# Optimization experiments

Hardware: AMD Instinct MI355X
Metric: run time of the kernel (lower is better)

The kernel has to match this reference:

```python
import jax, jax.numpy as jnp
import numpy as np

KS, AS = 13, 12  # kernel_size (12 vertices + center), anchor_size (icosahedron vertices)


def _icosa():
    # Icosahedron oriented with vertex 0 on +z (required by sort_level_vs xy-rotation logic)
    r5 = np.sqrt(5.0); rr = 2.0 / r5
    vs = [[0.0, 0.0, 1.0]]
    for k in range(5):
        t = 2.0 * np.pi * k / 5.0
        vs.append([rr * np.cos(t), rr * np.sin(t), 1.0 / r5])
    for k in range(5):
        t = 2.0 * np.pi * k / 5.0 + np.pi / 5.0
        vs.append([rr * np.cos(t), rr * np.sin(t), -1.0 / r5])
    vs.append([0.0, 0.0, -1.0])
    return np.array(vs)


def _rotm(axis, ang):
    a = np.asarray(axis, dtype=np.float64); a = a / np.linalg.norm(a)
    K = np.array([[0, -a[2], a[1]], [a[2], 0, -a[0]], [-a[1], a[0], 0]])
    return np.eye(3) + np.sin(ang) * K + (1.0 - np.cos(ang)) * (K @ K)


def _ico_group(vs):
    # Generate the 60-element icosahedral rotation group by closure from two generators
    gens = [_rotm([0.0, 0.0, 1.0], 2 * np.pi / 5), _rotm(vs[1], 2 * np.pi / 5)]
    group = [np.eye(3)]
    keys = {tuple(np.round(np.eye(3), 4).ravel())}
    frontier = [np.eye(3)]
    while frontier:
        nxt = []
        for g in frontier:
            for h in gens:
                c = h @ g
                k = tuple(np.round(c, 4).ravel())
                if k not in keys:
                    keys.add(k); group.append(c); nxt.append(c)
        frontier = nxt
    return group


def _sort_level_vs(v_idxs, vs):
    # Faithful port of sort_level_vs: order ring vertices by successive 72-deg xy rotations
    out = [v_idxs[0]]
    vs_l = vs[v_idxs][:, :2]
    cur = vs_l[[0]]
    dth = 2 * np.pi / 5
    R = np.array([[np.cos(dth), -np.sin(dth)], [np.sin(dth), np.cos(dth)]])
    for _ in range(4):
        cur = R.dot(cur.T).T
        out.append(v_idxs[np.argmin(np.abs(vs_l - cur).sum(1))])
    return np.array(out)


def _build_buffers():
    vs = _icosa()
    dots = vs @ vs.T
    v0_adjs = np.where(np.abs(dots[0] - 1.0 / np.sqrt(5)) < 1e-6)[0]
    v0_lv2 = np.where(np.abs(dots[0] + 1.0 / np.sqrt(5)) < 1e-6)[0]
    v0_opp = int(np.argmin(dots[0]))
    # 12 rotation anchors: one group element mapping vertex 0 to each vertex
    group = _ico_group(vs)
    vRs = []
    for i in range(12):
        for R in group:
            if np.linalg.norm(R @ vs[0] - vs[i]) < 1e-5:
                vRs.append(R); break
    vRs = np.stack(vRs)  # [12,3,3]
    rot_v = np.einsum('rij,aj->rai', vRs, vs)  # [12,12,3]
    d = np.linalg.norm(rot_v[:, :, None, :] - vs[None, None], axis=-1)
    trace_idx_ori = np.argmin(d, axis=2)  # [12,12] vertex permutation per anchor rotation
    trace_idx_rot = np.empty_like(trace_idx_ori)
    for r in range(12):
        trace_idx_rot[r, trace_idx_ori[r]] = np.arange(12)
    trace_idxv_rot = np.concatenate([trace_idx_rot, np.full((12, 1), 12, np.int64)], axis=1)  # [12,13]
    # idx_map: faithful port of the __init__ construction (maps 13*12 slots -> 36 weight params)
    inv = np.empty(12, np.int64)
    inv[0] = 0; inv[v0_adjs] = 1; inv[v0_lv2] = 2; inv[v0_opp] = 3
    a_s = _sort_level_vs(v0_adjs, vs)
    l_s = _sort_level_vs(v0_lv2, vs)
    idx_map = np.empty(KS * AS, np.int64)
    idx_map[:AS] = inv
    idx_map[v0_opp * AS:(v0_opp + 1) * AS] = inv + 4
    idx_map[-AS:] = inv + 8
    seq1 = np.arange(12, 24); seq2 = np.arange(24, 36)
    idx_map[a_s[0] * AS:(a_s[0] + 1) * AS] = seq1
    idx_map[l_s[0] * AS:(l_s[0] + 1) * AS] = seq2
    shifts = [[4, 0, 1, 2, 3], [3, 4, 0, 1, 2], [2, 3, 4, 0, 1], [1, 2, 3, 4, 0]]
    for j, sh in enumerate(shifts, start=1):
        new = np.empty(12, np.int64)
        new[a_s] = a_s[sh]; new[l_s] = l_s[sh]
        new[0] = 0; new[v0_opp] = v0_opp
        idx_map[a_s[j] * AS:(a_s[j] + 1) * AS] = seq1[new]
        idx_map[l_s[j] * AS:(l_s[j] + 1) * AS] = seq2[new]
    return idx_map, trace_idxv_rot, trace_idx_rot


def setup_inputs() -> dict:
    key = jax.random.key(0)
    k1, k2 = jax.random.split(key)
    B, CIN, COUT, P = 8, 16, 16, 4096
    x = jax.random.normal(k1, (B, CIN, KS, P, AS), dtype=jnp.float32)
    W = jax.random.normal(k2, (COUT, CIN, 36), dtype=jnp.float32) * 0.05  # xavier-scale
    idx_map, tivr, tir = _build_buffers()
    return {
        'x': x,
        'W': W,
        'idx_map': jnp.asarray(idx_map, jnp.int32),
        'trace_idxv_rot': jnp.asarray(tivr, jnp.int32),
        'trace_idx_rot': jnp.asarray(tir, jnp.int32),
    }


def reference(x, W, idx_map, trace_idxv_rot, trace_idx_rot):
    d_out, d_in, _ = W.shape
    # Expand 36 free params to the [d, c, k, a] kernel via idx_map gather
    Wm = W[:, :, idx_map].reshape(d_out, d_in, KS, AS)
    # The two torch.gather calls (dims 2 then 3) collapse to:
    # Wfull[d,c,k,a,r] = Wm[d,c, trace_idxv_rot[r,k], trace_idx_rot[r,a]]
    Wfull = Wm[:, :, trace_idxv_rot[:, :, None], trace_idx_rot[:, None, :]]  # [d,c,r,k,a]
    return jnp.einsum('dcrka,bckpa->bdpr', Wfull, x)
```

## Files before the change

### kernel.cpp

```cpp
#include <hip/hip_runtime.h>

#define B_    8
#define CIN_  16
#define COUT_ 16
#define KS_   13
#define AS_   12
#define P_    4096
#define R_    12
#define M_    192
#define KTOT  2496
#define BN    128
#define KT    96
#define NSTEP 26
#define LDP   104

typedef float  f32x4  __attribute__((ext_vector_type(4)));
typedef __bf16 bf16x4 __attribute__((ext_vector_type(4)));
typedef __bf16 bf16x8 __attribute__((ext_vector_type(8)));

__global__ void build_wmatf(const float* __restrict__ W,
                            const int* __restrict__ idx_map,
                            const int* __restrict__ tivr,
                            const int* __restrict__ tir,
                            __bf16* __restrict__ WmatF) {
  int gid  = blockIdx.x * blockDim.x + threadIdx.x;
  int lane = gid & 63;
  int fid  = gid >> 6;
  int kt   = fid / 36;
  int rem  = fid - kt * 36;
  int mt   = rem / 3;
  int ks   = rem - mt * 3;

  int row = mt * 16 + (lane & 15);
  int d = row / R_;
  int r = row - d * R_;

  bf16x8 v;
#pragma unroll
  for (int e = 0; e < 8; ++e) {
    int kap = kt * KT + ks * 32 + (lane >> 4) * 8 + e;
    int c = kap / (KS_ * AS_);
    int t = kap - c * (KS_ * AS_);
    int k = t / AS_;
    int a = t - k * AS_;
    int s = idx_map[tivr[r * KS_ + k] * AS_ + tir[r * AS_ + a]];
    v[e] = (__bf16)W[(d * CIN_ + c) * 36 + s];
  }
  *(bf16x8*)(WmatF + (size_t)gid * 8) = v;
}

__global__ __launch_bounds__(512, 2)
void s2conv(const float* __restrict__ x,
            const __bf16* __restrict__ WmatF,
            float* __restrict__ out) {
  __shared__ __bf16 Xs[2][BN][LDP];

  const int tid  = threadIdx.x;
  const int lane = tid & 63;
  const int wave = tid >> 6;
  const int wm   = wave >> 2;
  const int wn   = wave & 3;
  const int l15  = lane & 15;
  const int l4   = lane >> 4;

  const int wg = blockIdx.x;
  const int b  = wg >> 5;
  const int p0 = (wg & 31) << 7;

  f32x4 acc[6][2];
#pragma unroll
  for (int i = 0; i < 6; ++i)
#pragma unroll
    for (int j = 0; j < 2; ++j)
      acc[i][j] = f32x4{0.f, 0.f, 0.f, 0.f};

  auto load_x = [&](int kt, f32x4 (&st)[6]) {
    int ck = kt * 8 + wave;
    const f32x4* bp =
        (const f32x4*)(x + (size_t)(b * 208 + ck) * 49152 + (size_t)p0 * 12);
#pragma unroll
    for (int it = 0; it < 6; ++it) st[it] = bp[it * 64 + lane];
  };

  auto load_a = [&](int kt, bf16x8 (&af)[18]) {
    const char* base = (const char*)WmatF +
        (size_t)(kt * 36 + wm * 18) * 1024 + lane * 16;
#pragma unroll
    for (int f = 0; f < 18; ++f)
      af[f] = *(const bf16x8*)(base + f * 1024);
  };

  auto write_X = [&](int buf, f32x4 (&st)[6]) {
    char* xsb = (char*)&Xs[buf][0][0];
#pragma unroll
    for (int it = 0; it < 6; ++it) {
      int f4i = it * 64 + lane;
      int pl  = f4i / 3;
      int a   = (f4i - pl * 3) * 4;
      bf16x4 v = __builtin_convertvector(st[it], bf16x4);
      *(bf16x4*)(xsb + pl * (LDP * 2) + (wave * 12 + a) * 2) = v;
    }
  };

  auto mfma_step = [&](int buf, bf16x8 (&af)[18]) {
    const __bf16* xsb = &Xs[buf][0][0];
#pragma unroll
    for (int ks = 0; ks < 3; ++ks) {
      const int col = ks * 32 + l4 * 8;
      bf16x8 bfr[2];
#pragma unroll
      for (int nt = 0; nt < 2; ++nt)
        bfr[nt] = *(const bf16x8*)(xsb + (wn * 32 + nt * 16 + l15) * LDP + col);
#pragma unroll
      for (int mt = 0; mt < 6; ++mt)
#pragma unroll
        for (int nt = 0; nt < 2; ++nt)
          acc[mt][nt] = __builtin_amdgcn_mfma_f32_16x16x32_bf16(
              af[mt * 3 + ks], bfr[nt], acc[mt][nt], 0, 0, 0);
    }
  };

  auto barrier = [&]() {
    asm volatile("s_waitcnt lgkmcnt(0)" ::: "memory");
    __builtin_amdgcn_s_barrier();
  };

  f32x4  stA[6], stB[6];
  bf16x8 af[18];
  load_x(0, stA);
  load_x(1, stB);
  write_X(0, stA);
  barrier();

  for (int kt = 0; kt < NSTEP - 2; kt += 2) {
    load_a(kt, af);
    load_x(kt + 2, stA);
    __builtin_amdgcn_sched_barrier(0);
    write_X(1, stB);
    mfma_step(0, af);
    barrier();

    load_a(kt + 1, af);
    load_x(kt + 3, stB);
    __builtin_amdgcn_sched_barrier(0);
    write_X(0, stA);
    mfma_step(1, af);
    barrier();
  }

  load_a(24, af);
  write_X(1, stB);
  mfma_step(0, af);
  barrier();
  load_a(25, af);
  mfma_step(1, af);

#pragma unroll
  for (int mt = 0; mt < 6; ++mt) {
    int mrow0 = wm * 96 + mt * 16 + l4 * 4;
    int d  = mrow0 / 12;
    int r0 = mrow0 - d * 12;
#pragma unroll
    for (int nt = 0; nt < 2; ++nt) {
      int p = p0 + wn * 32 + nt * 16 + l15;
      float* dst = out + (size_t)((b * 16 + d) * 4096 + p) * 12 + r0;
      *(f32x4*)dst = acc[mt][nt];
    }
  }
}

extern "C" void kernel_launch(void* const* d_in, const int* in_sizes, int n_in,
                              void* d_out, int out_size, void* d_ws, size_t ws_size,
                              hipStream_t stream) {
  const float* x       = (const float*)d_in[0];
  const float* W       = (const float*)d_in[1];
  const int*   idx_map = (const int*)d_in[2];
  const int*   tivr    = (const int*)d_in[3];
  const int*   tir     = (const int*)d_in[4];
  float*       out     = (float*)d_out;
  __bf16*      WmatF   = (__bf16*)d_ws;

  build_wmatf<<<dim3(117), dim3(512), 0, stream>>>(W, idx_map, tivr, tir, WmatF);
  s2conv<<<dim3(256), dim3(512), 0, stream>>>(x, WmatF, out);
}
```

Baseline: 82.35 us.

## Stage weights into LDS via global_load_lds and feed x directly from registers

The dataflow is reversed. Weight fragments are now staged into shared memory with direct global-to-LDS loads, double-buffered across K steps. Each wave reads its x fragments straight from global memory into registers and converts them to bf16 in place, which removes the x LDS transpose and write. Each wave owns 16 pixels and all 192 output rows (12 accumulators). The cost is uncoalesced-ish 16-byte x loads with a large stride and more LDS reads of A per MFMA.

```diff
diff --git a/kernel.cpp b/kernel.cpp
--- a/kernel.cpp
+++ b/kernel.cpp
@@ -1,22 +1,22 @@
 #include <hip/hip_runtime.h>
+#include <stdint.h>
 
-#define B_    8
 #define CIN_  16
-#define COUT_ 16
 #define KS_   13
 #define AS_   12
-#define P_    4096
 #define R_    12
-#define M_    192
-#define KTOT  2496
-#define BN    128
 #define KT    96
 #define NSTEP 26
-#define LDP   104
 
 typedef float  f32x4  __attribute__((ext_vector_type(4)));
 typedef __bf16 bf16x4 __attribute__((ext_vector_type(4)));
 typedef __bf16 bf16x8 __attribute__((ext_vector_type(8)));
+
+__device__ static inline void gll16(const void* g, void* l) {
+  __builtin_amdgcn_global_load_lds(
+      (const __attribute__((address_space(1))) uint32_t*)g,
+      (__attribute__((address_space(3))) uint32_t*)l, 16, 0, 0);
+}
 
 __global__ void build_wmatf(const float* __restrict__ W,
                             const int* __restrict__ idx_map,
@@ -28,8 +28,8 @@
   int fid  = gid >> 6;
   int kt   = fid / 36;
   int rem  = fid - kt * 36;
-  int mt   = rem / 3;
-  int ks   = rem - mt * 3;
+  int ks   = rem / 12;
+  int mt   = rem - ks * 12;
 
   int row = mt * 16 + (lane & 15);
   int d = row / R_;
@@ -53,119 +53,116 @@
 void s2conv(const float* __restrict__ x,
             const __bf16* __restrict__ WmatF,
             float* __restrict__ out) {
-  __shared__ __bf16 Xs[2][BN][LDP];
+  __shared__ __bf16 As[2][36 * 512];
 
   const int tid  = threadIdx.x;
   const int lane = tid & 63;
   const int wave = tid >> 6;
-  const int wm   = wave >> 2;
-  const int wn   = wave & 3;
   const int l15  = lane & 15;
   const int l4   = lane >> 4;
 
   const int wg = blockIdx.x;
   const int b  = wg >> 5;
   const int p0 = (wg & 31) << 7;
+  const int p  = p0 + wave * 16 + l15;
 
-  f32x4 acc[6][2];
+  int voff[3][2];
 #pragma unroll
-  for (int i = 0; i < 6; ++i)
+  for (int ks = 0; ks < 3; ++ks)
 #pragma unroll
-    for (int j = 0; j < 2; ++j)
-      acc[i][j] = f32x4{0.f, 0.f, 0.f, 0.f};
+    for (int h = 0; h < 2; ++h) {
+      int kl = ks * 32 + l4 * 8 + h * 4;
+      int ck = kl / 12, a = kl - ck * 12;
+      voff[ks][h] = (ck * 49152 + a + p * 12) * 4;
+    }
+  const char* xb = (const char*)(x + (size_t)b * 208 * 49152);
 
-  auto load_x = [&](int kt, f32x4 (&st)[6]) {
-    int ck = kt * 8 + wave;
-    const f32x4* bp =
-        (const f32x4*)(x + (size_t)(b * 208 + ck) * 49152 + (size_t)p0 * 12);
+  f32x4 acc[12];
 #pragma unroll
-    for (int it = 0; it < 6; ++it) st[it] = bp[it * 64 + lane];
+  for (int i = 0; i < 12; ++i) acc[i] = f32x4{0.f, 0.f, 0.f, 0.f};
+
+  const int fr0 = wave * 4;
+  const int fr4 = 32 + (wave & 3);
+
+  auto stageA = [&](int kt, int buf) {
+    const char* gk = (const char*)WmatF + (size_t)kt * 36864;
+    char* lb = (char*)&As[buf][0];
+#pragma unroll
+    for (int f = 0; f < 4; ++f) {
+      int frag = fr0 + f;
+      gll16(gk + frag * 1024 + lane * 16, lb + frag * 1024);
+    }
+    gll16(gk + fr4 * 1024 + lane * 16, lb + fr4 * 1024);
   };
 
-  auto load_a = [&](int kt, bf16x8 (&af)[18]) {
-    const char* base = (const char*)WmatF +
-        (size_t)(kt * 36 + wm * 18) * 1024 + lane * 16;
+  auto loadB = [&](int kt, f32x4 (&bs)[3][2]) {
+    const char* xk = xb + (size_t)kt * (8 * 49152 * 4);
 #pragma unroll
-    for (int f = 0; f < 18; ++f)
-      af[f] = *(const bf16x8*)(base + f * 1024);
+    for (int ks = 0; ks < 3; ++ks)
+#pragma unroll
+      for (int h = 0; h < 2; ++h)
+        bs[ks][h] = *(const f32x4*)(xk + voff[ks][h]);
   };
 
-  auto write_X = [&](int buf, f32x4 (&st)[6]) {
-    char* xsb = (char*)&Xs[buf][0][0];
+  auto mfma_phase = [&](int buf, f32x4 (&bs)[3][2]) {
+    const char* lb = (const char*)&As[buf][0];
 #pragma unroll
-    for (int it = 0; it < 6; ++it) {
-      int f4i = it * 64 + lane;
-      int pl  = f4i / 3;
-      int a   = (f4i - pl * 3) * 4;
-      bf16x4 v = __builtin_convertvector(st[it], bf16x4);
-      *(bf16x4*)(xsb + pl * (LDP * 2) + (wave * 12 + a) * 2) = v;
+    for (int ks = 0; ks < 3; ++ks) {
+      bf16x4 lo = __builtin_convertvector(bs[ks][0], bf16x4);
+      bf16x4 hi = __builtin_convertvector(bs[ks][1], bf16x4);
+      bf16x8 bfr = __builtin_shufflevector(lo, hi, 0, 1, 2, 3, 4, 5, 6, 7);
+#pragma unroll
+      for (int mt = 0; mt < 12; ++mt) {
+        bf16x8 af = *(const bf16x8*)(lb + (ks * 12 + mt) * 1024 + lane * 16);
+        acc[mt] = __builtin_amdgcn_mfma_f32_16x16x32_bf16(af, bfr, acc[mt],
+                                                          0, 0, 0);
+      }
     }
   };
 
-  auto mfma_step = [&](int buf, bf16x8 (&af)[18]) {
-    const __bf16* xsb = &Xs[buf][0][0];
-#pragma unroll
-    for (int ks = 0; ks < 3; ++ks) {
-      const int col = ks * 32 + l4 * 8;
-      bf16x8 bfr[2];
-#pragma unroll
-      for (int nt = 0; nt < 2; ++nt)
-        bfr[nt] = *(const bf16x8*)(xsb + (wn * 32 + nt * 16 + l15) * LDP + col);
-#pragma unroll
-      for (int mt = 0; mt < 6; ++mt)
-#pragma unroll
-        for (int nt = 0; nt < 2; ++nt)
-          acc[mt][nt] = __builtin_amdgcn_mfma_f32_16x16x32_bf16(
-              af[mt * 3 + ks], bfr[nt], acc[mt][nt], 0, 0, 0);
-    }
-  };
+  f32x4 bsE[3][2], bsO[3][2];
 
-  auto barrier = [&]() {
-    asm volatile("s_waitcnt lgkmcnt(0)" ::: "memory");
+  stageA(0, 0);
+  __builtin_amdgcn_sched_barrier(0);
+  loadB(0, bsE);
+  __builtin_amdgcn_sched_barrier(0);
+  asm volatile("s_waitcnt vmcnt(6)" ::: "memory");
+  __builtin_amdgcn_s_barrier();
+
+#pragma unroll 1
+  for (int j = 0; j < 24; j += 2) {
+    stageA(j + 1, 1);
+    __builtin_amdgcn_sched_barrier(0);
+    loadB(j + 1, bsO);
+    __builtin_amdgcn_sched_barrier(0);
+    mfma_phase(0, bsE);
+    asm volatile("s_waitcnt vmcnt(6)" ::: "memory");
     __builtin_amdgcn_s_barrier();
-  };
 
-  f32x4  stA[6], stB[6];
-  bf16x8 af[18];
-  load_x(0, stA);
-  load_x(1, stB);
-  write_X(0, stA);
-  barrier();
-
-  for (int kt = 0; kt < NSTEP - 2; kt += 2) {
-    load_a(kt, af);
-    load_x(kt + 2, stA);
+    stageA(j + 2, 0);
     __builtin_amdgcn_sched_barrier(0);
-    write_X(1, stB);
-    mfma_step(0, af);
-    barrier();
-
-    load_a(kt + 1, af);
-    load_x(kt + 3, stB);
+    loadB(j + 2, bsE);
     __builtin_amdgcn_sched_barrier(0);
-    write_X(0, stA);
-    mfma_step(1, af);
-    barrier();
+    mfma_phase(1, bsO);
+    asm volatile("s_waitcnt vmcnt(6)" ::: "memory");
+    __builtin_amdgcn_s_barrier();
   }
-
-  load_a(24, af);
-  write_X(1, stB);
-  mfma_step(0, af);
-  barrier();
-  load_a(25, af);
-  mfma_step(1, af);
+  stageA(25, 1);
+  __builtin_amdgcn_sched_barrier(0);
+  loadB(25, bsO);
+  __builtin_amdgcn_sched_barrier(0);
+  mfma_phase(0, bsE);
+  asm volatile("s_waitcnt vmcnt(6)" ::: "memory");
+  __builtin_amdgcn_s_barrier();
+  mfma_phase(1, bsO);
 
 #pragma unroll
-  for (int mt = 0; mt < 6; ++mt) {
-    int mrow0 = wm * 96 + mt * 16 + l4 * 4;
+  for (int mt = 0; mt < 12; ++mt) {
+    int mrow0 = mt * 16 + l4 * 4;
     int d  = mrow0 / 12;
     int r0 = mrow0 - d * 12;
-#pragma unroll
-    for (int nt = 0; nt < 2; ++nt) {
-      int p = p0 + wn * 32 + nt * 16 + l15;
-      float* dst = out + (size_t)((b * 16 + d) * 4096 + p) * 12 + r0;
-      *(f32x4*)dst = acc[mt][nt];
-    }
+    float* dst = out + (size_t)((b * 16 + d) * 4096 + p) * 12 + r0;
+    *(f32x4*)dst = acc[mt];
   }
 }
 
```

New measurement: 78.11 us. 1.05x faster.

## Shrink GEMM tile to 64 points with 4 waves and double-buffered A fragments

Applied to the files above, without the earlier changes.

The main kernel now uses 256-thread blocks, each covering 64 points over all 192 output rows, and launches 512 blocks instead of 256. Each wave owns 48 rows and 4 column tiles, so every wave reads the whole B tile from LDS. The weight fragments are now double-buffered in registers (even/odd sets) so A loads for the next step overlap the current MFMAs. build_wmatf reorders its fragment layout to match the new per-wave A loads. The intent is better occupancy, more blocks across the CUs and lower A-load latency, at the cost of less reuse of each A fragment per block and more A traffic per point.

```diff
diff --git a/kernel.cpp b/kernel.cpp
--- a/kernel.cpp
+++ b/kernel.cpp
@@ -1,15 +1,10 @@
 #include <hip/hip_runtime.h>
+#include <stdint.h>
 
-#define B_    8
 #define CIN_  16
-#define COUT_ 16
 #define KS_   13
 #define AS_   12
-#define P_    4096
 #define R_    12
-#define M_    192
-#define KTOT  2496
-#define BN    128
 #define KT    96
 #define NSTEP 26
 #define LDP   104
@@ -28,8 +23,11 @@
   int fid  = gid >> 6;
   int kt   = fid / 36;
   int rem  = fid - kt * 36;
-  int mt   = rem / 3;
-  int ks   = rem - mt * 3;
+  int w    = rem / 9;
+  int sub  = rem - w * 9;
+  int mtl  = sub / 3;
+  int ks   = sub - mtl * 3;
+  int mt   = w * 3 + mtl;
 
   int row = mt * 16 + (lane & 15);
   int d = row / R_;
@@ -49,74 +47,80 @@
   *(bf16x8*)(WmatF + (size_t)gid * 8) = v;
 }
 
-__global__ __launch_bounds__(512, 2)
+__global__ __launch_bounds__(256, 2)
 void s2conv(const float* __restrict__ x,
             const __bf16* __restrict__ WmatF,
             float* __restrict__ out) {
-  __shared__ __bf16 Xs[2][BN][LDP];
+  __shared__ __bf16 Xs[2][64][LDP];
 
   const int tid  = threadIdx.x;
   const int lane = tid & 63;
   const int wave = tid >> 6;
-  const int wm   = wave >> 2;
-  const int wn   = wave & 3;
   const int l15  = lane & 15;
   const int l4   = lane >> 4;
 
   const int wg = blockIdx.x;
-  const int b  = wg >> 5;
-  const int p0 = (wg & 31) << 7;
+  const int b  = wg >> 6;
+  const int p0 = (wg & 63) << 6;
 
-  f32x4 acc[6][2];
+  f32x4 acc[3][4];
 #pragma unroll
-  for (int i = 0; i < 6; ++i)
+  for (int i = 0; i < 3; ++i)
 #pragma unroll
-    for (int j = 0; j < 2; ++j)
+    for (int j = 0; j < 4; ++j)
       acc[i][j] = f32x4{0.f, 0.f, 0.f, 0.f};
 
-  auto load_x = [&](int kt, f32x4 (&st)[6]) {
-    int ck = kt * 8 + wave;
-    const f32x4* bp =
-        (const f32x4*)(x + (size_t)(b * 208 + ck) * 49152 + (size_t)p0 * 12);
+  const char* aBase = (const char*)WmatF + (size_t)wave * 9216 + lane * 16;
+  auto loadA = [&](int kt, bf16x8 (&af)[9]) {
+    const char* gk = aBase + (size_t)kt * 36864;
 #pragma unroll
-    for (int it = 0; it < 6; ++it) st[it] = bp[it * 64 + lane];
+    for (int f = 0; f < 9; ++f)
+      af[f] = *(const bf16x8*)(gk + f * 1024);
   };
 
-  auto load_a = [&](int kt, bf16x8 (&af)[18]) {
-    const char* base = (const char*)WmatF +
-        (size_t)(kt * 36 + wm * 18) * 1024 + lane * 16;
+  const char* xb = (const char*)x + ((size_t)b * 208) * 49152 * 4
+                   + (size_t)p0 * 48;
+  auto load_x = [&](int kt, f32x4 (&st)[6]) {
 #pragma unroll
-    for (int f = 0; f < 18; ++f)
-      af[f] = *(const bf16x8*)(base + f * 1024);
+    for (int h = 0; h < 2; ++h) {
+      const char* bp = xb + ((size_t)(kt * 8 + wave * 2 + h)) * (49152 * 4);
+#pragma unroll
+      for (int j = 0; j < 3; ++j)
+        st[h * 3 + j] = *(const f32x4*)(bp + (j * 64 + lane) * 16);
+    }
   };
 
   auto write_X = [&](int buf, f32x4 (&st)[6]) {
     char* xsb = (char*)&Xs[buf][0][0];
 #pragma unroll
-    for (int it = 0; it < 6; ++it) {
-      int f4i = it * 64 + lane;
-      int pl  = f4i / 3;
-      int a   = (f4i - pl * 3) * 4;
-      bf16x4 v = __builtin_convertvector(st[it], bf16x4);
-      *(bf16x4*)(xsb + pl * (LDP * 2) + (wave * 12 + a) * 2) = v;
+    for (int h = 0; h < 2; ++h) {
+      int ck12 = (wave * 2 + h) * 12;
+#pragma unroll
+      for (int j = 0; j < 3; ++j) {
+        int f4i = j * 64 + lane;
+        int pl  = f4i / 3;
+        int a   = (f4i - pl * 3) * 4;
+        bf16x4 v = __builtin_convertvector(st[h * 3 + j], bf16x4);
+        *(bf16x4*)(xsb + (pl * LDP + ck12 + a) * 2) = v;
+      }
     }
   };
 
-  auto mfma_step = [&](int buf, bf16x8 (&af)[18]) {
+  auto mfma_phase = [&](int buf, bf16x8 (&af)[9]) {
     const __bf16* xsb = &Xs[buf][0][0];
 #pragma unroll
     for (int ks = 0; ks < 3; ++ks) {
-      const int col = ks * 32 + l4 * 8;
-      bf16x8 bfr[2];
+      bf16x8 bfr[4];
 #pragma unroll
-      for (int nt = 0; nt < 2; ++nt)
-        bfr[nt] = *(const bf16x8*)(xsb + (wn * 32 + nt * 16 + l15) * LDP + col);
+      for (int nt = 0; nt < 4; ++nt)
+        bfr[nt] = *(const bf16x8*)(xsb + (nt * 16 + l15) * LDP
+                                       + ks * 32 + l4 * 8);
 #pragma unroll
-      for (int mt = 0; mt < 6; ++mt)
+      for (int mtl = 0; mtl < 3; ++mtl)
 #pragma unroll
-        for (int nt = 0; nt < 2; ++nt)
-          acc[mt][nt] = __builtin_amdgcn_mfma_f32_16x16x32_bf16(
-              af[mt * 3 + ks], bfr[nt], acc[mt][nt], 0, 0, 0);
+        for (int nt = 0; nt < 4; ++nt)
+          acc[mtl][nt] = __builtin_amdgcn_mfma_f32_16x16x32_bf16(
+              af[mtl * 3 + ks], bfr[nt], acc[mtl][nt], 0, 0, 0);
     }
   };
 
@@ -125,46 +129,49 @@
     __builtin_amdgcn_s_barrier();
   };
 
-  f32x4  stA[6], stB[6];
-  bf16x8 af[18];
-  load_x(0, stA);
-  load_x(1, stB);
-  write_X(0, stA);
+  f32x4  s0[6], s1[6];
+  bf16x8 aE[9], aO[9];
+  load_x(0, s0);
+  load_x(1, s1);
+  loadA(0, aE);
+  __builtin_amdgcn_sched_barrier(0);
+  write_X(0, s0);
   barrier();
 
-  for (int kt = 0; kt < NSTEP - 2; kt += 2) {
-    load_a(kt, af);
-    load_x(kt + 2, stA);
+#pragma unroll 1
+  for (int t = 0; t < 24; t += 2) {
+    load_x(t + 2, s0);
+    loadA(t + 1, aO);
     __builtin_amdgcn_sched_barrier(0);
-    write_X(1, stB);
-    mfma_step(0, af);
+    write_X(1, s1);
+    mfma_phase(0, aE);
     barrier();
 
-    load_a(kt + 1, af);
-    load_x(kt + 3, stB);
+    load_x(t + 3, s1);
+    loadA(t + 2, aE);
     __builtin_amdgcn_sched_barrier(0);
-    write_X(0, stA);
-    mfma_step(1, af);
+    write_X(0, s0);
+    mfma_phase(1, aO);
     barrier();
   }
 
-  load_a(24, af);
-  write_X(1, stB);
-  mfma_step(0, af);
+  loadA(25, aO);
+  __builtin_amdgcn_sched_barrier(0);
+  write_X(1, s1);
+  mfma_phase(0, aE);
   barrier();
-  load_a(25, af);
-  mfma_step(1, af);
+  mfma_phase(1, aO);
 
 #pragma unroll
-  for (int mt = 0; mt < 6; ++mt) {
-    int mrow0 = wm * 96 + mt * 16 + l4 * 4;
+  for (int mtl = 0; mtl < 3; ++mtl) {
+    int mrow0 = wave * 48 + mtl * 16 + l4 * 4;
     int d  = mrow0 / 12;
     int r0 = mrow0 - d * 12;
 #pragma unroll
-    for (int nt = 0; nt < 2; ++nt) {
-      int p = p0 + wn * 32 + nt * 16 + l15;
+    for (int nt = 0; nt < 4; ++nt) {
+      int p = p0 + nt * 16 + l15;
       float* dst = out + (size_t)((b * 16 + d) * 4096 + p) * 12 + r0;
-      *(f32x4*)dst = acc[mt][nt];
+      *(f32x4*)dst = acc[mtl][nt];
     }
   }
 }
@@ -181,5 +188,5 @@
   __bf16*      WmatF   = (__bf16*)d_ws;
 
   build_wmatf<<<dim3(117), dim3(512), 0, stream>>>(W, idx_map, tivr, tir, WmatF);
-  s2conv<<<dim3(256), dim3(512), 0, stream>>>(x, WmatF, out);
+  s2conv<<<dim3(512), dim3(256), 0, stream>>>(x, WmatF, out);
 }
```

Result: no change. 80.99 us (-1.6%).
